# Kernel tuning notes

Hardware: AMD Instinct MI355X
Metric: run time of the kernel (lower is better)

The kernel has to match this reference:

```python
import jax, jax.numpy as jnp
import numpy as np

D_MODEL = 1024
STATE_DIM = 16
BATCH = 32
SEQ = 2048


def setup_inputs() -> dict:
    key = jax.random.key(0)
    k_x, k_win, k_bin, k_wout, k_bout = jax.random.split(key, 5)
    proj_dim = 2 * D_MODEL + 3 * STATE_DIM
    x = jax.random.normal(k_x, (BATCH, SEQ, D_MODEL), dtype=jnp.float32)
    # Dense kernels (glorot-ish scale) and zero biases, as in fresh keras layers
    W_in = jax.random.normal(k_win, (D_MODEL, proj_dim), dtype=jnp.float32) * 0.02
    b_in = jnp.zeros((proj_dim,), dtype=jnp.float32)
    W_out = jax.random.normal(k_wout, (D_MODEL, D_MODEL), dtype=jnp.float32) * 0.02
    b_out = jnp.zeros((D_MODEL,), dtype=jnp.float32)
    # A_log init: -log([1..state_dim])
    A_log = -jnp.log(jnp.arange(1, STATE_DIM + 1, dtype=jnp.float32))
    return {"x": x, "W_in": W_in, "b_in": b_in, "A_log": A_log,
            "W_out": W_out, "b_out": b_out}


def _selective_scan(delta, A, B, C):
    # delta, B, C: [b, s, n]; A: [n]
    # state_t = exp(A * delta_t) * state_{t-1} + B_t ; y_t = sum(state_t * C_t)
    def step(state, inp):
        delta_t, B_t, C_t = inp  # each [b, n]
        state = jnp.exp(A * delta_t) * state + B_t
        y = jnp.sum(state * C_t, axis=-1)  # [b]
        return state, y

    b = delta.shape[0]
    init = jnp.zeros((b, A.shape[0]), dtype=delta.dtype)
    # scan over time: move seq axis to front -> [s, b, n]
    xs = (jnp.swapaxes(delta, 0, 1), jnp.swapaxes(B, 0, 1), jnp.swapaxes(C, 0, 1))
    _, ys = jax.lax.scan(step, init, xs)  # ys: [s, b]
    return jnp.swapaxes(ys, 0, 1)  # [b, s]


def reference(x, W_in, b_in, A_log, W_out, b_out):
    xz = jnp.einsum('bsd,dp->bsp', x, W_in) + b_in  # [b, s, 2*d + 3*n]
    d, n = D_MODEL, STATE_DIM
    xm = xz[..., :d]                     # unused by scan (matches original)
    z = xz[..., d:2 * d]                 # [b, s, d]
    Bm = xz[..., 2 * d:2 * d + n]        # [b, s, n]
    Cm = xz[..., 2 * d + n:2 * d + 2 * n]
    delta = jax.nn.softplus(xz[..., 2 * d + 2 * n:])  # [b, s, n]
    A = -jnp.exp(A_log)                  # [n]
    y = _selective_scan(delta, A, Bm, Cm)  # [b, s]
    y = y[..., None] * jax.nn.gelu(z, approximate=False)  # [b, s, d]
    return jnp.einsum('bsd,de->bse', y, W_out) + b_out
```

## Files before the change

kernel.cpp:

```cpp
#include <hip/hip_runtime.h>
#include <cstdint>

typedef float fx4 __attribute__((ext_vector_type(4)));
typedef short sx8 __attribute__((ext_vector_type(8)));
typedef short sx4 __attribute__((ext_vector_type(4)));

#define NSTATE 16
#define SEQ_LEN 2048
#define NBATCH 32
#define MROWS 65536
#define KDIM 1024
#define N1 1072
#define N1PAD 1152
#define BK 32
#define NSTEP (KDIM / BK)
#define TILE_SHORTS 4096
#define TSTRIDE (NSTEP * TILE_SHORTS)
#define RING 4
#define SLOT_SHORTS 8192

__device__ __forceinline__ short f2bf(float f) {
  unsigned u = __float_as_uint(f);
  u += 0x7FFFu + ((u >> 16) & 1u);
  return (short)(u >> 16);
}

__device__ __forceinline__ float gelu_exact(float x) {
  float ax = fabsf(x) * 0.70710678118654752f;
  float t = __builtin_amdgcn_rcpf(fmaf(0.3275911f, ax, 1.0f));
  float p = fmaf(1.061405429f, t, -1.453152027f);
  p = fmaf(p, t, 1.421413741f);
  p = fmaf(p, t, -0.284496736f);
  p = fmaf(p, t, 0.254829592f);
  p = p * t;
  float e = __expf(-ax * ax);
  float erfv = fmaf(-p, e, 1.0f);
  erfv = copysignf(erfv, x);
  return 0.5f * x * (1.0f + erfv);
}

#define GLOAD_LDS16(gp, lp)                                                          \
  __builtin_amdgcn_global_load_lds(                                                  \
      (const __attribute__((address_space(1))) unsigned int*)(gp),                   \
      (__attribute__((address_space(3))) unsigned int*)(lp), 16, 0, 0)

#define SBAR() do { __builtin_amdgcn_s_barrier(); asm volatile("" ::: "memory"); } while (0)

__global__ void convert_pack_x(const float* __restrict__ x, short* __restrict__ xbp) {
  const int wave = threadIdx.x >> 6;
  const int lane = threadIdx.x & 63;
  const int r0 = blockIdx.x * 64 + wave * 16;
  const int q = (lane & 7) >> 1;
  const int eo = (lane & 1) * 4;
  const int kt0 = lane >> 3;
  for (int r16 = 0; r16 < 16; ++r16) {
    const int m = r0 + r16;
    const int rloc = m & 127;
    const long pbase = ((long)(m >> 7) * NSTEP) * TILE_SHORTS + rloc * 32;
    const int p8 = (((q + (rloc >> 1)) & 3)) * 8 + eo;
#pragma unroll
    for (int seg = 0; seg < 4; ++seg) {
      fx4 v = *(const fx4*)(x + (long)m * KDIM + seg * 256 + lane * 4);
      sx4 o;
      o[0] = f2bf(v[0]); o[1] = f2bf(v[1]); o[2] = f2bf(v[2]); o[3] = f2bf(v[3]);
      *(sx4*)(xbp + pbase + (long)(seg * 8 + kt0) * TILE_SHORTS + p8) = o;
    }
  }
}

__global__ void transpose_w_kernel(const float* __restrict__ src, short* __restrict__ dst,
                                   int src_cols, int col_off, int valid_rows) {
  __shared__ float t[32][33];
  int j0 = blockIdx.x * 32;
  int k0 = blockIdx.y * 32;
  int c = threadIdx.x & 31;
  int r = threadIdx.x >> 5;
#pragma unroll
  for (int i = 0; i < 4; i++) {
    int k = k0 + r + i * 8;
    int j = j0 + c;
    float v = (j < valid_rows) ? src[(long)k * src_cols + col_off + j] : 0.f;
    t[r + i * 8][c] = v;
  }
  __syncthreads();
#pragma unroll
  for (int i = 0; i < 4; i++) {
    int n = j0 + r + i * 8;
    int k = k0 + c;
    int rr = n & 127;
    long addr = ((long)(n >> 7) * NSTEP + (k >> 5)) * TILE_SHORTS + rr * 32
              + ((((k >> 3) & 3) + ((rr >> 1) & 3)) & 3) * 8 + (k & 7);
    dst[addr] = f2bf(t[c][r + i * 8]);
  }
}

__device__ __forceinline__ void gemm_mainloop256(const short* __restrict__ Abase,
                                                 const short* __restrict__ Bbase,
                                                 short* lds, fx4 acc[4][4]) {
  const int tid = threadIdx.x;
  const int lane = tid & 63;
  const int wave = tid >> 6;
  const int wm = wave >> 2, wn = wave & 3;
  const int l15 = lane & 15, ks = lane >> 4;

#pragma unroll
  for (int i = 0; i < 4; i++)
#pragma unroll
    for (int j = 0; j < 4; j++) acc[i][j] = fx4{0.f, 0.f, 0.f, 0.f};

  short* AshR = lds;
  short* BshR = lds + RING * SLOT_SHORTS;
  const short* Asrc = Abase + (long)(tid >> 9) * TSTRIDE + (tid & 511) * 8;
  const short* Bsrc = Bbase + (long)(tid >> 9) * TSTRIDE + (tid & 511) * 8;
  const int dst = tid * 8;

  const int rslot = ((ks + (l15 >> 1)) & 3) * 8;
  const int aoff = (wm >> 1) * TILE_SHORTS + ((wm & 1) * 64 + l15) * 32 + rslot;
  const int boff = (wn >> 1) * TILE_SHORTS + ((wn & 1) * 64 + l15) * 32 + rslot;

#pragma unroll
  for (int s = 0; s < RING - 1; s++) {
    GLOAD_LDS16(Asrc + (long)s * TILE_SHORTS, AshR + s * SLOT_SHORTS + dst);
    GLOAD_LDS16(Bsrc + (long)s * TILE_SHORTS, BshR + s * SLOT_SHORTS + dst);
  }

  for (int s = 0; s < NSTEP; ++s) {
    const int rem = NSTEP - 1 - s;
    if (rem >= 2)      asm volatile("s_waitcnt vmcnt(4)" ::: "memory");
    else if (rem == 1) asm volatile("s_waitcnt vmcnt(2)" ::: "memory");
    else               asm volatile("s_waitcnt vmcnt(0)" ::: "memory");
    SBAR();

    if (s + 3 < NSTEP) {
      const int sl = (s + 3) & (RING - 1);
      GLOAD_LDS16(Asrc + (long)(s + 3) * TILE_SHORTS, AshR + sl * SLOT_SHORTS + dst);
      GLOAD_LDS16(Bsrc + (long)(s + 3) * TILE_SHORTS, BshR + sl * SLOT_SHORTS + dst);
    }

    const short* sa = AshR + (s & (RING - 1)) * SLOT_SHORTS + aoff;
    const short* sb = BshR + (s & (RING - 1)) * SLOT_SHORTS + boff;
    sx8 af[4], bfr[4];
#pragma unroll
    for (int i = 0; i < 4; i++) af[i] = *(const sx8*)(sa + i * 512);
#pragma unroll
    for (int j = 0; j < 4; j++) bfr[j] = *(const sx8*)(sb + j * 512);
    asm volatile("s_waitcnt lgkmcnt(0)" ::: "memory");
    __builtin_amdgcn_sched_barrier(0);

    __builtin_amdgcn_s_setprio(1);
#pragma unroll
    for (int i = 0; i < 4; i++)
#pragma unroll
      for (int j = 0; j < 4; j++)
        acc[i][j] = __builtin_amdgcn_mfma_f32_16x16x32_bf16(af[i], bfr[j], acc[i][j], 0, 0, 0);
    __builtin_amdgcn_s_setprio(0);
  }
}

__global__ __launch_bounds__(1024, 1) void gemm1_kernel(
    const short* __restrict__ xbp, const short* __restrict__ Wt1p,
    const float* __restrict__ b_in, short* __restrict__ g) {
  extern __shared__ short lds[];
  const int bid = blockIdx.x;
  const int wgid = (bid & 7) * 128 + (bid >> 3);
  const int nt = wgid & 3;
  const int mt = wgid >> 2;
  fx4 acc[4][4];
  gemm_mainloop256(xbp + (long)(mt * 2) * TSTRIDE,
                   Wt1p + (long)(nt * 2) * TSTRIDE, lds, acc);

  const int lane = threadIdx.x & 63;
  const int wave = threadIdx.x >> 6;
  const int wm = wave >> 2, wn = wave & 3;
  const int m0 = mt * 256;
  const int n0 = nt * 256;

#pragma unroll
  for (int ni = 0; ni < 4; ni++) {
    int n = n0 + wn * 64 + ni * 16 + (lane & 15);
    float bias = b_in[1024 + n];
#pragma unroll
    for (int mi = 0; mi < 4; mi++) {
#pragma unroll
      for (int r = 0; r < 4; r++) {
        int m = m0 + wm * 64 + mi * 16 + (lane >> 4) * 4 + r;
        float v = acc[mi][ni][r] + bias;
        int rr = m & 127;
        long addr = ((long)(m >> 7) * NSTEP + (n >> 5)) * TILE_SHORTS + rr * 32
                  + ((((n >> 3) & 3) + ((rr >> 1) & 3)) & 3) * 8 + (n & 7);
        g[addr] = f2bf(gelu_exact(v));
      }
    }
  }
}

__global__ __launch_bounds__(256, 2) void gemm_bcd_kernel(
    const short* __restrict__ xbp, const short* __restrict__ Wt1p,
    const float* __restrict__ b_in, const float* __restrict__ A_log,
    float* __restrict__ Bb, float* __restrict__ Cb, float* __restrict__ ab) {
  __shared__ short Ash[3 * 4096] __attribute__((aligned(16)));
  __shared__ short Bsh[3 * 2048] __attribute__((aligned(16)));
  const int tid = threadIdx.x;
  const int lane = tid & 63, wave = tid >> 6;
  const int l15 = lane & 15, ks = lane >> 4;
  const int bid = blockIdx.x;
  const int mt = (bid & 7) * 64 + (bid >> 3);
  const short* Abase = xbp + (long)mt * TSTRIDE;
  const short* Bbase = Wt1p + (long)8 * TSTRIDE;

  fx4 acc[2][3];
#pragma unroll
  for (int i = 0; i < 2; i++)
#pragma unroll
    for (int j = 0; j < 3; j++) acc[i][j] = fx4{0.f, 0.f, 0.f, 0.f};

  const int rslot = ((ks + (l15 >> 1)) & 3) * 8;
  const int aofb = (wave * 32 + l15) * 32 + rslot;

#pragma unroll
  for (int s = 0; s < 2; s++) {
    GLOAD_LDS16(Abase + (long)s * TILE_SHORTS + tid * 8, Ash + s * 4096 + tid * 8);
    GLOAD_LDS16(Abase + (long)s * TILE_SHORTS + 2048 + tid * 8, Ash + s * 4096 + 2048 + tid * 8);
    GLOAD_LDS16(Bbase + (long)s * TILE_SHORTS + tid * 8, Bsh + s * 2048 + tid * 8);
  }

  for (int s = 0; s < NSTEP; ++s) {
    if (s < NSTEP - 1) asm volatile("s_waitcnt vmcnt(3)" ::: "memory");
    else               asm volatile("s_waitcnt vmcnt(0)" ::: "memory");
    SBAR();
    if (s + 2 < NSTEP) {
      const int sl = (s + 2) % 3;
      GLOAD_LDS16(Abase + (long)(s + 2) * TILE_SHORTS + tid * 8, Ash + sl * 4096 + tid * 8);
      GLOAD_LDS16(Abase + (long)(s + 2) * TILE_SHORTS + 2048 + tid * 8, Ash + sl * 4096 + 2048 + tid * 8);
      GLOAD_LDS16(Bbase + (long)(s + 2) * TILE_SHORTS + tid * 8, Bsh + sl * 2048 + tid * 8);
    }
    const short* sa = Ash + (s % 3) * 4096 + aofb;
    const short* sb = Bsh + (s % 3) * 2048;
    sx8 af[2], bfr[3];
#pragma unroll
    for (int i = 0; i < 2; i++) af[i] = *(const sx8*)(sa + i * 512);
#pragma unroll
    for (int j = 0; j < 3; j++) bfr[j] = *(const sx8*)(sb + (j * 16 + l15) * 32 + rslot);
    asm volatile("s_waitcnt lgkmcnt(0)" ::: "memory");
    __builtin_amdgcn_sched_barrier(0);
#pragma unroll
    for (int i = 0; i < 2; i++)
#pragma unroll
      for (int j = 0; j < 3; j++)
        acc[i][j] = __builtin_amdgcn_mfma_f32_16x16x32_bf16(af[i], bfr[j], acc[i][j], 0, 0, 0);
  }

  const float biasB = b_in[2048 + l15];
  const float biasC = b_in[2064 + l15];
  const float biasD = b_in[2080 + l15];
  const float Ac = -expf(A_log[l15]);
#pragma unroll
  for (int mi = 0; mi < 2; mi++) {
#pragma unroll
    for (int r = 0; r < 4; r++) {
      int m = mt * 128 + wave * 32 + mi * 16 + (lane >> 4) * 4 + r;
      Bb[m * NSTATE + l15] = acc[mi][0][r] + biasB;
      Cb[m * NSTATE + l15] = acc[mi][1][r] + biasC;
      float v = acc[mi][2][r] + biasD;
      float dlt = (v > 20.f) ? v : log1pf(expf(v));
      ab[m * NSTATE + l15] = expf(Ac * dlt);
    }
  }
}

__global__ void scan_kernel(const float* __restrict__ ab, const float* __restrict__ Bb,
                            const float* __restrict__ Cb, float* __restrict__ p) {
  int b = blockIdx.x;
  int ln = threadIdx.x;
  if (ln >= NSTATE) return;
  const float* pa = ab + b * SEQ_LEN * NSTATE + ln;
  const float* pb = Bb + b * SEQ_LEN * NSTATE + ln;
  const float* pc = Cb + b * SEQ_LEN * NSTATE + ln;
  float* po = p + (long)b * SEQ_LEN * NSTATE + ln;
  float s = 0.f;
  float a0[8], b0[8], c0[8], a1[8], b1[8], c1[8];
#pragma unroll
  for (int u = 0; u < 8; u++) {
    int o = u * NSTATE;
    a0[u] = pa[o]; b0[u] = pb[o]; c0[u] = pc[o];
  }
  for (int t0 = 0; t0 < SEQ_LEN; t0 += 16) {
#pragma unroll
    for (int u = 0; u < 8; u++) {
      int o = (t0 + 8 + u) * NSTATE;
      a1[u] = pa[o]; b1[u] = pb[o]; c1[u] = pc[o];
    }
#pragma unroll
    for (int u = 0; u < 8; u++) {
      s = fmaf(a0[u], s, b0[u]);
      po[(t0 + u) * NSTATE] = s * c0[u];
    }
    if (t0 + 16 < SEQ_LEN) {
#pragma unroll
      for (int u = 0; u < 8; u++) {
        int o = (t0 + 16 + u) * NSTATE;
        a0[u] = pa[o]; b0[u] = pb[o]; c0[u] = pc[o];
      }
    }
#pragma unroll
    for (int u = 0; u < 8; u++) {
      s = fmaf(a1[u], s, b1[u]);
      po[(t0 + 8 + u) * NSTATE] = s * c1[u];
    }
  }
}

__global__ void reduce_y_kernel(const float* __restrict__ p, float* __restrict__ y) {
  int m = blockIdx.x * blockDim.x + threadIdx.x;
  const fx4* row = (const fx4*)(p + (long)m * NSTATE);
  fx4 v = row[0] + row[1] + row[2] + row[3];
  y[m] = v[0] + v[1] + v[2] + v[3];
}

__global__ __launch_bounds__(1024, 1) void gemm2_kernel(
    const short* __restrict__ g, const short* __restrict__ Wt2p,
    const float* __restrict__ y, const float* __restrict__ b_out,
    float* __restrict__ out) {
  extern __shared__ short lds[];
  const int bid = blockIdx.x;
  const int wgid = (bid & 7) * 128 + (bid >> 3);
  const int nt = wgid & 3;
  const int mt = wgid >> 2;
  fx4 acc[4][4];
  gemm_mainloop256(g + (long)(mt * 2) * TSTRIDE,
                   Wt2p + (long)(nt * 2) * TSTRIDE, lds, acc);

  const int lane = threadIdx.x & 63;
  const int wave = threadIdx.x >> 6;
  const int wm = wave >> 2, wn = wave & 3;
  const int m0 = mt * 256;
  const int n0 = nt * 256;

#pragma unroll
  for (int mi = 0; mi < 4; mi++) {
#pragma unroll
    for (int r = 0; r < 4; r++) {
      int m = m0 + wm * 64 + mi * 16 + (lane >> 4) * 4 + r;
      float ym = y[m];
#pragma unroll
      for (int ni = 0; ni < 4; ni++) {
        int n = n0 + wn * 64 + ni * 16 + (lane & 15);
        out[(long)m * 1024 + n] = fmaf(ym, acc[mi][ni][r], b_out[n]);
      }
    }
  }
}

extern "C" void kernel_launch(void* const* d_in, const int* in_sizes, int n_in,
                              void* d_out, int out_size, void* d_ws, size_t ws_size,
                              hipStream_t stream) {
  const float* x     = (const float*)d_in[0];
  const float* W_in  = (const float*)d_in[1];
  const float* b_in  = (const float*)d_in[2];
  const float* A_log = (const float*)d_in[3];
  const float* W_out = (const float*)d_in[4];
  const float* b_out = (const float*)d_in[5];
  float* out = (float*)d_out;

  char* ws = (char*)d_ws;
  short* xbp = (short*)ws;  ws += (size_t)MROWS * KDIM * 2;
  short* g   = (short*)ws;  ws += (size_t)MROWS * KDIM * 2;
  short* Wt1p = (short*)ws; ws += (size_t)N1PAD * KDIM * 2;
  short* Wt2p = (short*)ws; ws += (size_t)KDIM * KDIM * 2;
  float* Bb = (float*)ws;  ws += (size_t)MROWS * NSTATE * 4;
  float* Cb = (float*)ws;  ws += (size_t)MROWS * NSTATE * 4;
  float* ab = (float*)ws;  ws += (size_t)MROWS * NSTATE * 4;
  float* p  = (float*)ws;  ws += (size_t)MROWS * NSTATE * 4;
  float* y  = (float*)ws;  ws += (size_t)MROWS * 4;

  const int ldsBytes = 2 * RING * SLOT_SHORTS * 2;

  convert_pack_x<<<1024, 256, 0, stream>>>(x, xbp);
  transpose_w_kernel<<<dim3(N1PAD / 32, 32), 256, 0, stream>>>(W_in, Wt1p, 2096, 1024, N1);
  transpose_w_kernel<<<dim3(32, 32), 256, 0, stream>>>(W_out, Wt2p, 1024, 0, 1024);
  gemm_bcd_kernel<<<512, 256, 0, stream>>>(xbp, Wt1p, b_in, A_log, Bb, Cb, ab);
  scan_kernel<<<NBATCH, 64, 0, stream>>>(ab, Bb, Cb, p);
  reduce_y_kernel<<<MROWS / 256, 256, 0, stream>>>(p, y);
  gemm1_kernel<<<1024, 1024, ldsBytes, stream>>>(xbp, Wt1p, b_in, g);
  gemm2_kernel<<<1024, 1024, ldsBytes, stream>>>(g, Wt2p, y, b_out, out);
}
```

Baseline: 519.9 us.

## Chunk-parallel scan with fused reduction and LDS-staged vectorized GEMM epilogues

```diff
diff --git a/kernel.cpp b/kernel.cpp
--- a/kernel.cpp
+++ b/kernel.cpp
@@ -45,6 +45,7 @@
       (__attribute__((address_space(3))) unsigned int*)(lp), 16, 0, 0)
 
 #define SBAR() do { __builtin_amdgcn_s_barrier(); asm volatile("" ::: "memory"); } while (0)
+#define WAITLGKM0() asm volatile("s_waitcnt lgkmcnt(0)" ::: "memory")
 
 __global__ void convert_pack_x(const float* __restrict__ x, short* __restrict__ xbp) {
   const int wave = threadIdx.x >> 6;
@@ -144,7 +145,7 @@
     for (int i = 0; i < 4; i++) af[i] = *(const sx8*)(sa + i * 512);
 #pragma unroll
     for (int j = 0; j < 4; j++) bfr[j] = *(const sx8*)(sb + j * 512);
-    asm volatile("s_waitcnt lgkmcnt(0)" ::: "memory");
+    WAITLGKM0();
     __builtin_amdgcn_sched_barrier(0);
 
     __builtin_amdgcn_s_setprio(1);
@@ -172,25 +173,39 @@
   const int lane = threadIdx.x & 63;
   const int wave = threadIdx.x >> 6;
   const int wm = wave >> 2, wn = wave & 3;
+  const int l15 = lane & 15, ks = lane >> 4;
   const int m0 = mt * 256;
   const int n0 = nt * 256;
 
-#pragma unroll
-  for (int ni = 0; ni < 4; ni++) {
-    int n = n0 + wn * 64 + ni * 16 + (lane & 15);
-    float bias = b_in[1024 + n];
-#pragma unroll
-    for (int mi = 0; mi < 4; mi++) {
-#pragma unroll
-      for (int r = 0; r < 4; r++) {
-        int m = m0 + wm * 64 + mi * 16 + (lane >> 4) * 4 + r;
-        float v = acc[mi][ni][r] + bias;
-        int rr = m & 127;
-        long addr = ((long)(m >> 7) * NSTEP + (n >> 5)) * TILE_SHORTS + rr * 32
-                  + ((((n >> 3) & 3) + ((rr >> 1) & 3)) & 3) * 8 + (n & 7);
-        g[addr] = f2bf(gelu_exact(v));
+  SBAR();
+  float* cst = (float*)lds;
+  const fx4 bi = *(const fx4*)(b_in + 1024 + n0 + lane * 4);
+  const int kcol = n0 + lane * 4;
+  for (int s = 0; s < 16; ++s) {
+    if (wm == (s >> 2)) {
+      const int mi = s & 3;
+#pragma unroll
+      for (int ni = 0; ni < 4; ni++) {
+        int c = wn * 64 + ni * 16 + l15;
+#pragma unroll
+        for (int r = 0; r < 4; r++)
+          cst[(ks * 4 + r) * 257 + c] = acc[mi][ni][r];
       }
     }
+    WAITLGKM0();
+    SBAR();
+    {
+      const int m = m0 + s * 16 + wave;
+      fx4 v = *(const fx4*)(cst + wave * 257 + lane * 4);
+      sx4 o;
+#pragma unroll
+      for (int i = 0; i < 4; i++) o[i] = f2bf(gelu_exact(v[i] + bi[i]));
+      const int rr = m & 127;
+      long addr = ((long)(m >> 7) * NSTEP + (kcol >> 5)) * TILE_SHORTS + rr * 32
+                + ((((kcol >> 3) & 3) + ((rr >> 1) & 3)) & 3) * 8 + (kcol & 7);
+      *(sx4*)(g + addr) = o;
+    }
+    SBAR();
   }
 }
 
@@ -241,7 +256,7 @@
     for (int i = 0; i < 2; i++) af[i] = *(const sx8*)(sa + i * 512);
 #pragma unroll
     for (int j = 0; j < 3; j++) bfr[j] = *(const sx8*)(sb + (j * 16 + l15) * 32 + rslot);
-    asm volatile("s_waitcnt lgkmcnt(0)" ::: "memory");
+    WAITLGKM0();
     __builtin_amdgcn_sched_barrier(0);
 #pragma unroll
     for (int i = 0; i < 2; i++)
@@ -269,52 +284,58 @@
 }
 
 __global__ void scan_kernel(const float* __restrict__ ab, const float* __restrict__ Bb,
-                            const float* __restrict__ Cb, float* __restrict__ p) {
-  int b = blockIdx.x;
-  int ln = threadIdx.x;
-  if (ln >= NSTATE) return;
-  const float* pa = ab + b * SEQ_LEN * NSTATE + ln;
-  const float* pb = Bb + b * SEQ_LEN * NSTATE + ln;
-  const float* pc = Cb + b * SEQ_LEN * NSTATE + ln;
-  float* po = p + (long)b * SEQ_LEN * NSTATE + ln;
-  float s = 0.f;
-  float a0[8], b0[8], c0[8], a1[8], b1[8], c1[8];
-#pragma unroll
-  for (int u = 0; u < 8; u++) {
-    int o = u * NSTATE;
-    a0[u] = pa[o]; b0[u] = pb[o]; c0[u] = pc[o];
-  }
-  for (int t0 = 0; t0 < SEQ_LEN; t0 += 16) {
+                            const float* __restrict__ Cb, float* __restrict__ y) {
+  __shared__ float Ash[16][17], Bsh[16][17];
+  const int b = blockIdx.x;
+  const int tid = threadIdx.x;
+  const int seg = tid >> 4, ch = tid & 15;
+  const long base = ((long)b * SEQ_LEN + seg * 128) * NSTATE + ch;
+  const float* pa = ab + base;
+  const float* pb = Bb + base;
+  const float* pc = Cb + base;
+
+  float A = 1.f, Bc = 0.f;
+  for (int i0 = 0; i0 < 128; i0 += 8) {
+    float av[8], bv[8];
+#pragma unroll
+    for (int u = 0; u < 8; u++) { av[u] = pa[(i0 + u) * NSTATE]; bv[u] = pb[(i0 + u) * NSTATE]; }
+#pragma unroll
+    for (int u = 0; u < 8; u++) { Bc = fmaf(av[u], Bc, bv[u]); A *= av[u]; }
+  }
+  Ash[seg][ch] = A; Bsh[seg][ch] = Bc;
+  __syncthreads();
+
+  if (tid < 16) {
+    float s = 0.f;
+    for (int sg = 0; sg < 16; ++sg) {
+      float nxt = fmaf(Ash[sg][tid], s, Bsh[sg][tid]);
+      Bsh[sg][tid] = s;
+      s = nxt;
+    }
+  }
+  __syncthreads();
+
+  float s = Bsh[seg][ch];
+  float* py = y + (long)b * SEQ_LEN + seg * 128;
+  for (int i0 = 0; i0 < 128; i0 += 8) {
+    float av[8], bv[8], cv[8];
 #pragma unroll
     for (int u = 0; u < 8; u++) {
-      int o = (t0 + 8 + u) * NSTATE;
-      a1[u] = pa[o]; b1[u] = pb[o]; c1[u] = pc[o];
+      av[u] = pa[(i0 + u) * NSTATE];
+      bv[u] = pb[(i0 + u) * NSTATE];
+      cv[u] = pc[(i0 + u) * NSTATE];
     }
 #pragma unroll
     for (int u = 0; u < 8; u++) {
-      s = fmaf(a0[u], s, b0[u]);
-      po[(t0 + u) * NSTATE] = s * c0[u];
-    }
-    if (t0 + 16 < SEQ_LEN) {
-#pragma unroll
-      for (int u = 0; u < 8; u++) {
-        int o = (t0 + 16 + u) * NSTATE;
-        a0[u] = pa[o]; b0[u] = pb[o]; c0[u] = pc[o];
-      }
-    }
-#pragma unroll
-    for (int u = 0; u < 8; u++) {
-      s = fmaf(a1[u], s, b1[u]);
-      po[(t0 + 8 + u) * NSTATE] = s * c1[u];
-    }
-  }
-}
-
-__global__ void reduce_y_kernel(const float* __restrict__ p, float* __restrict__ y) {
-  int m = blockIdx.x * blockDim.x + threadIdx.x;
-  const fx4* row = (const fx4*)(p + (long)m * NSTATE);
-  fx4 v = row[0] + row[1] + row[2] + row[3];
-  y[m] = v[0] + v[1] + v[2] + v[3];
+      s = fmaf(av[u], s, bv[u]);
+      float p = s * cv[u];
+      p += __shfl_xor(p, 1);
+      p += __shfl_xor(p, 2);
+      p += __shfl_xor(p, 4);
+      p += __shfl_xor(p, 8);
+      if (ch == 0) py[i0 + u] = p;
+    }
+  }
 }
 
 __global__ __launch_bounds__(1024, 1) void gemm2_kernel(
@@ -333,21 +354,36 @@
   const int lane = threadIdx.x & 63;
   const int wave = threadIdx.x >> 6;
   const int wm = wave >> 2, wn = wave & 3;
+  const int l15 = lane & 15, ks = lane >> 4;
   const int m0 = mt * 256;
   const int n0 = nt * 256;
 
-#pragma unroll
-  for (int mi = 0; mi < 4; mi++) {
-#pragma unroll
-    for (int r = 0; r < 4; r++) {
-      int m = m0 + wm * 64 + mi * 16 + (lane >> 4) * 4 + r;
-      float ym = y[m];
+  SBAR();
+  float* cst = (float*)lds;
+  const fx4 bo = *(const fx4*)(b_out + n0 + lane * 4);
+  for (int s = 0; s < 16; ++s) {
+    if (wm == (s >> 2)) {
+      const int mi = s & 3;
 #pragma unroll
       for (int ni = 0; ni < 4; ni++) {
-        int n = n0 + wn * 64 + ni * 16 + (lane & 15);
-        out[(long)m * 1024 + n] = fmaf(ym, acc[mi][ni][r], b_out[n]);
+        int c = wn * 64 + ni * 16 + l15;
+#pragma unroll
+        for (int r = 0; r < 4; r++)
+          cst[(ks * 4 + r) * 257 + c] = acc[mi][ni][r];
       }
     }
+    WAITLGKM0();
+    SBAR();
+    {
+      const int m = m0 + s * 16 + wave;
+      const float ym = y[m];
+      fx4 v = *(const fx4*)(cst + wave * 257 + lane * 4);
+      fx4 o;
+#pragma unroll
+      for (int i = 0; i < 4; i++) o[i] = fmaf(ym, v[i], bo[i]);
+      *(fx4*)(out + (long)m * 1024 + n0 + lane * 4) = o;
+    }
+    SBAR();
   }
 }
 
@@ -370,7 +406,6 @@
   float* Bb = (float*)ws;  ws += (size_t)MROWS * NSTATE * 4;
   float* Cb = (float*)ws;  ws += (size_t)MROWS * NSTATE * 4;
   float* ab = (float*)ws;  ws += (size_t)MROWS * NSTATE * 4;
-  float* p  = (float*)ws;  ws += (size_t)MROWS * NSTATE * 4;
   float* y  = (float*)ws;  ws += (size_t)MROWS * 4;
 
   const int ldsBytes = 2 * RING * SLOT_SHORTS * 2;
@@ -379,8 +414,7 @@
   transpose_w_kernel<<<dim3(N1PAD / 32, 32), 256, 0, stream>>>(W_in, Wt1p, 2096, 1024, N1);
   transpose_w_kernel<<<dim3(32, 32), 256, 0, stream>>>(W_out, Wt2p, 1024, 0, 1024);
   gemm_bcd_kernel<<<512, 256, 0, stream>>>(xbp, Wt1p, b_in, A_log, Bb, Cb, ab);
-  scan_kernel<<<NBATCH, 64, 0, stream>>>(ab, Bb, Cb, p);
-  reduce_y_kernel<<<MROWS / 256, 256, 0, stream>>>(p, y);
+  scan_kernel<<<NBATCH, 256, 0, stream>>>(ab, Bb, Cb, y);
   gemm1_kernel<<<1024, 1024, ldsBytes, stream>>>(xbp, Wt1p, b_in, g);
   gemm2_kernel<<<1024, 1024, ldsBytes, stream>>>(g, Wt2p, y, b_out, out);
 }
```

After: 507.4 us. -2.4%, faster.
